# Kernel optimization log

Hardware: AMD Instinct MI355X
Metric: run time of the kernel (lower is better)

The kernel has to match this reference:

```python
import jax, jax.numpy as jnp
import numpy as np

N, EN, NNZ, D, H = 100000, 25000, 200000, 128, 4
F = D  # out_channels per head (out_channels == embed_dim)
NEG_SLOPE = 0.2


def segment_softmax(logits, seg, num_segments):
    # numerically stable softmax over entries sharing the same segment id
    m = jax.ops.segment_max(logits, seg, num_segments=num_segments)
    ex = jnp.exp(logits - m[seg])
    s = jax.ops.segment_sum(ex, seg, num_segments=num_segments)
    return ex / s[seg]


def setup_inputs():
    key = jax.random.key(0)
    ks = jax.random.split(key, 10)
    X = jax.random.normal(ks[0], (N, D), jnp.float32)
    E = jax.random.normal(ks[1], (EN, D), jnp.float32)
    row = jax.random.randint(ks[2], (NNZ,), 0, N, dtype=jnp.int32)
    col = (jnp.arange(NNZ, dtype=jnp.int32) % EN)  # every hyperedge non-empty
    adj_index = jnp.stack([row, col])  # [2, nnz]
    adj_values = jax.random.uniform(ks[3], (NNZ,), jnp.float32) + 0.1
    s = 1.0 / np.sqrt(D)
    Wn = jax.random.normal(ks[4], (D, D), jnp.float32) * s
    bn = jnp.zeros((D,), jnp.float32)
    We = jax.random.normal(ks[5], (D, D), jnp.float32) * s
    be = jnp.zeros((D,), jnp.float32)
    Wlin = jax.random.normal(ks[6], (D, H * F), jnp.float32) * s
    att = jax.random.normal(ks[7], (1, H, 2 * F), jnp.float32) * s
    bias_conv = jnp.zeros((F,), jnp.float32)
    return {"X": X, "E": E, "adj_index": adj_index, "adj_values": adj_values,
            "Wn": Wn, "bn": bn, "We": We, "be": be, "Wlin": Wlin,
            "att": att, "bias_conv": bias_conv}


def reference(X, E, adj_index, adj_values, Wn, bn, We, be, Wlin, att, bias_conv):
    row, col = adj_index[0], adj_index[1]  # node idx, hyperedge idx

    # ---- compute_edge_feat: E_res = B^{-1} A^T (X Wn + bn) + (E We + be) + E
    edge_deg = jax.ops.segment_sum(adj_values, col, num_segments=EN)  # tsp.sum(A,0)
    norm_factor = 1.0 / edge_deg  # edges guaranteed non-empty
    X_trans = X @ Wn + bn
    agg = jax.ops.segment_sum(adj_values[:, None] * X_trans[row], col, num_segments=EN)
    E_res = norm_factor[:, None] * agg + (E @ We + be) + E

    # ---- HypergraphConv(use_attention=True, heads=H, concat=False), eval (dropout off)
    x = (X @ Wlin).reshape(N, H, F)
    e = (E_res @ Wlin).reshape(EN, H, F)
    x_i = x[row]           # [nnz, H, F]
    e_j = e[col]           # [nnz, H, F]
    alpha = (x_i * att[:, :, :F]).sum(-1) + (e_j * att[:, :, F:]).sum(-1)  # [nnz, H]
    alpha = jax.nn.leaky_relu(alpha, NEG_SLOPE)
    alpha = segment_softmax(alpha, row, N)  # softmax grouped by node index

    # degree normalizations D (nodes) and B (hyperedges)
    Dn = jax.ops.segment_sum(adj_values[col], row, num_segments=N)
    Dn = jnp.where(Dn > 0, 1.0 / Dn, 0.0)
    Bn = jax.ops.segment_sum(jnp.ones((NNZ,), x.dtype), col, num_segments=EN)
    Bn = jnp.where(Bn > 0, 1.0 / Bn, 0.0)

    # node -> hyperedge aggregation
    m1 = Bn[col][:, None, None] * x_i * alpha[:, :, None]
    out_e = jax.ops.segment_sum(m1, col, num_segments=EN)  # [EN, H, F]
    # hyperedge -> node aggregation
    m2 = Dn[row][:, None, None] * out_e[col] * alpha[:, :, None]
    out_n = jax.ops.segment_sum(m2, row, num_segments=N)   # [N, H, F]

    X_res = out_n.mean(axis=1) + bias_conv  # concat=False -> mean over heads + bias
    return (X_res, E_res)
```

## Files before the change

kernel.cpp:

```cpp
#include <hip/hip_runtime.h>

#define NN 100000
#define ENUM 25000
#define NNZ_C 200000

typedef __attribute__((ext_vector_type(8))) short bf16x8;
typedef __attribute__((ext_vector_type(4))) float f32x4;

__device__ __forceinline__ float bf2f(unsigned short v) {
    return __uint_as_float(((unsigned)v) << 16);
}
__device__ __forceinline__ float blo(unsigned u) { return __uint_as_float(u << 16); }
__device__ __forceinline__ float bhi(unsigned u) { return __uint_as_float(u & 0xFFFF0000u); }
__device__ __forceinline__ unsigned short f2bf(float x) {
    unsigned u = __float_as_uint(x);
    unsigned r = (u + 0x7fff + ((u >> 16) & 1)) >> 16;
    return (unsigned short)r;
}
__device__ __forceinline__ unsigned pack2(float a, float b) {
    return (unsigned)f2bf(a) | ((unsigned)f2bf(b) << 16);
}
__device__ __forceinline__ void gload_lds16(const unsigned short* g, unsigned short* l) {
    __builtin_amdgcn_global_load_lds(
        (const __attribute__((address_space(1))) void*)g,
        (__attribute__((address_space(3))) void*)l, 16, 0, 0);
}

template <bool PERM>
__global__ __launch_bounds__(256) void wtr_k(
    const float* __restrict__ W, unsigned short* __restrict__ Wt, int NC)
{
    const int t = blockIdx.x * 256 + threadIdx.x;
    if (t >= 128 * NC) return;
    const int c = t % NC, k = t / NC;
    const int cc = PERM ? ((c & 127) * 4 + (c >> 7)) : c;
    const size_t pos = ((size_t)cc * 128 + k) ^ ((cc & 7) << 3);
    Wt[pos] = f2bf(W[t]);
}

__global__ __launch_bounds__(256) void attw_k(
    const float* __restrict__ Wlin, const float* __restrict__ att,
    float* __restrict__ A1, float* __restrict__ A2)
{
    const int t = threadIdx.x;
    const int k = t & 127;
    const int pair = t >> 7;
    const float* wrow = Wlin + (size_t)k * 512;
    float s[4];
    #pragma unroll
    for (int h = 0; h < 4; h++) {
        float acc = 0.f;
        const float* ap = att + h * 256 + pair * 128;
        const float* wp = wrow + h * 128;
        for (int f = 0; f < 128; f++) acc += wp[f] * ap[f];
        s[h] = acc;
    }
    float* dst = (pair ? A2 : A1) + k * 4;
    dst[0] = s[0]; dst[1] = s[1]; dst[2] = s[2]; dst[3] = s[3];
}

__global__ __launch_bounds__(256) void gemmx_k(
    const float* __restrict__ X, const unsigned short* __restrict__ Wc,
    const float* __restrict__ bn, const float* __restrict__ A1,
    unsigned short* __restrict__ Xt, unsigned short* __restrict__ Xlin,
    float* __restrict__ ax, int M)
{
    __shared__ unsigned short As[64 * 128];
    __shared__ unsigned short Bs[64 * 128];
    __shared__ float A1s[512];
    const int tid = threadIdx.x;
    const int r0 = blockIdx.x * 64;

    {
        int rr = tid >> 4;
        const int kc = (tid & 15) * 8;
        #pragma unroll
        for (int it = 0; it < 4; it++) {
            int r = r0 + rr; if (r > M - 1) r = M - 1;
            const float* ap = X + (size_t)r * 128 + kc;
            const float4 f0 = *(const float4*)ap;
            const float4 f1 = *(const float4*)(ap + 4);
            uint4 va;
            va.x = pack2(f0.x, f0.y); va.y = pack2(f0.z, f0.w);
            va.z = pack2(f1.x, f1.y); va.w = pack2(f1.z, f1.w);
            *(uint4*)&As[(rr * 128 + kc) ^ ((rr & 7) << 3)] = va;
            rr += 16;
        }
    }
    A1s[tid] = A1[tid];
    A1s[tid + 256] = A1[tid + 256];
    __syncthreads();

    {
        const int rr = tid >> 2;
        const int fq = (tid & 3) * 32;
        float s0 = 0.f, s1 = 0.f, s2 = 0.f, s3 = 0.f;
        #pragma unroll
        for (int i = 0; i < 32; i += 8) {
            const bf16x8 v = *(const bf16x8*)&As[(rr * 128 + fq + i) ^ ((rr & 7) << 3)];
            #pragma unroll
            for (int j = 0; j < 8; j++) {
                const float xv = bf2f((unsigned short)v[j]);
                const float* ap = A1s + (fq + i + j) * 4;
                s0 += xv * ap[0]; s1 += xv * ap[1];
                s2 += xv * ap[2]; s3 += xv * ap[3];
            }
        }
        s0 += __shfl_xor(s0, 1); s1 += __shfl_xor(s1, 1);
        s2 += __shfl_xor(s2, 1); s3 += __shfl_xor(s3, 1);
        s0 += __shfl_xor(s0, 2); s1 += __shfl_xor(s1, 2);
        s2 += __shfl_xor(s2, 2); s3 += __shfl_xor(s3, 2);
        const int r = r0 + rr;
        if ((tid & 3) == 0 && r < M)
            *(float4*)(ax + (size_t)r * 4) = make_float4(s0, s1, s2, s3);
    }

    const int lane = tid & 63;
    const int wid = tid >> 6;
    const int wr = wid >> 1, wc = wid & 1;
    const int fr = lane & 15;
    const int kg = (lane >> 4) * 8;

    bf16x8 a[2][4];
    #pragma unroll
    for (int m = 0; m < 2; m++) {
        const int ar = wr * 32 + m * 16 + fr;
        #pragma unroll
        for (int ks = 0; ks < 4; ks++)
            a[m][ks] = *(const bf16x8*)&As[(ar * 128 + ks * 32 + kg) ^ ((ar & 7) << 3)];
    }

    for (int ct = 0; ct < 10; ct++) {
        __syncthreads();
        {
            const unsigned short* src = Wc + (size_t)ct * 8192 + tid * 8;
            unsigned short* dst = &Bs[tid * 8];
            #pragma unroll
            for (int it = 0; it < 4; it++)
                gload_lds16(src + it * 2048, dst + it * 2048);
        }
        __syncthreads();

        f32x4 acc[2][2] = {};
        #pragma unroll
        for (int ks = 0; ks < 4; ks++) {
            bf16x8 b[2];
            #pragma unroll
            for (int n = 0; n < 2; n++) {
                const int br = wc * 32 + n * 16 + fr;
                b[n] = *(const bf16x8*)&Bs[(br * 128 + ks * 32 + kg) ^ ((br & 7) << 3)];
            }
            #pragma unroll
            for (int m = 0; m < 2; m++)
                #pragma unroll
                for (int n = 0; n < 2; n++)
                    acc[m][n] = __builtin_amdgcn_mfma_f32_16x16x32_bf16(a[m][ks], b[n], acc[m][n], 0, 0, 0);
        }

        #pragma unroll
        for (int m = 0; m < 2; m++) {
            #pragma unroll
            for (int n = 0; n < 2; n++) {
                const int ccol = wc * 32 + n * 16 + fr;
                #pragma unroll
                for (int j = 0; j < 4; j++) {
                    const int r = r0 + wr * 32 + m * 16 + (lane >> 4) * 4 + j;
                    if (r < M) {
                        const float v = acc[m][n][j];
                        if (ct < 2) {
                            const int c = ct * 64 + ccol;
                            Xt[(size_t)r * 128 + c] = f2bf(v + bn[c]);
                        } else {
                            const int c = (ct - 2) * 64 + ccol;
                            Xlin[(size_t)r * 512 + c] = f2bf(v);
                        }
                    }
                }
            }
        }
    }
}

template <bool BF16OUT, int CT, bool AF32>
__global__ __launch_bounds__(256) void gemm2_k(
    const void* __restrict__ Av, const unsigned short* __restrict__ Wt,
    const float* __restrict__ bias, const float* __restrict__ resid,
    void* __restrict__ Cv, int M)
{
    const int NC = CT * 64;
    __shared__ unsigned short As[64 * 128];
    __shared__ unsigned short Bs[64 * 128];
    const int tid = threadIdx.x;
    const int r0 = blockIdx.x * 64;

    {
        int rr = tid >> 4;
        const int kc = (tid & 15) * 8;
        #pragma unroll
        for (int it = 0; it < 4; it++) {
            int r = r0 + rr; if (r > M - 1) r = M - 1;
            uint4 va;
            if (AF32) {
                const float* ap = (const float*)Av + (size_t)r * 128 + kc;
                const float4 f0 = *(const float4*)ap;
                const float4 f1 = *(const float4*)(ap + 4);
                va.x = pack2(f0.x, f0.y); va.y = pack2(f0.z, f0.w);
                va.z = pack2(f1.x, f1.y); va.w = pack2(f1.z, f1.w);
            } else {
                va = *(const uint4*)((const unsigned short*)Av + (size_t)r * 128 + kc);
            }
            *(uint4*)&As[(rr * 128 + kc) ^ ((rr & 7) << 3)] = va;
            rr += 16;
        }
    }
    __syncthreads();

    const int lane = tid & 63;
    const int wid = tid >> 6;
    const int wr = wid >> 1, wc = wid & 1;
    const int fr = lane & 15;
    const int kg = (lane >> 4) * 8;

    bf16x8 a[2][4];
    #pragma unroll
    for (int m = 0; m < 2; m++) {
        const int ar = wr * 32 + m * 16 + fr;
        #pragma unroll
        for (int ks = 0; ks < 4; ks++)
            a[m][ks] = *(const bf16x8*)&As[(ar * 128 + ks * 32 + kg) ^ ((ar & 7) << 3)];
    }

    for (int ct = 0; ct < CT; ct++) {
        __syncthreads();
        {
            const unsigned short* src = Wt + (size_t)ct * 8192 + tid * 8;
            unsigned short* dst = &Bs[tid * 8];
            #pragma unroll
            for (int it = 0; it < 4; it++)
                gload_lds16(src + it * 2048, dst + it * 2048);
        }
        __syncthreads();

        f32x4 acc[2][2] = {};
        #pragma unroll
        for (int ks = 0; ks < 4; ks++) {
            bf16x8 b[2];
            #pragma unroll
            for (int n = 0; n < 2; n++) {
                const int br = wc * 32 + n * 16 + fr;
                b[n] = *(const bf16x8*)&Bs[(br * 128 + ks * 32 + kg) ^ ((br & 7) << 3)];
            }
            #pragma unroll
            for (int m = 0; m < 2; m++)
                #pragma unroll
                for (int n = 0; n < 2; n++)
                    acc[m][n] = __builtin_amdgcn_mfma_f32_16x16x32_bf16(a[m][ks], b[n], acc[m][n], 0, 0, 0);
        }

        const int c0 = ct * 64;
        #pragma unroll
        for (int m = 0; m < 2; m++) {
            #pragma unroll
            for (int n = 0; n < 2; n++) {
                const int c = c0 + wc * 32 + n * 16 + (lane & 15);
                #pragma unroll
                for (int j = 0; j < 4; j++) {
                    const int r = r0 + wr * 32 + m * 16 + (lane >> 4) * 4 + j;
                    if (r < M) {
                        float v = acc[m][n][j];
                        if (bias) v += bias[c];
                        if (resid) v += resid[(size_t)r * NC + c];
                        if (BF16OUT) ((unsigned short*)Cv)[(size_t)r * NC + c] = f2bf(v);
                        else         ((float*)Cv)[(size_t)r * NC + c] = v;
                    }
                }
            }
        }
    }
}

__global__ __launch_bounds__(256) void edge_agg_k(
    const int* __restrict__ row, const float* __restrict__ adjv,
    const unsigned short* __restrict__ Xt, const float* __restrict__ A2,
    float* __restrict__ Eres, float* __restrict__ ae)
{
    __shared__ float part[4][4];
    const int s = threadIdx.x >> 7;
    const int e = blockIdx.x * 2 + s;
    const int f = threadIdx.x & 127;
    float v = 0.f;
    if (e < ENUM) {
        float acc = 0.f, deg = 0.f;
        #pragma unroll
        for (int j = 0; j < 8; j++) {
            const int k = e + j * ENUM;
            const float w = adjv[k];
            deg += w;
            acc += w * blo(Xt[(size_t)row[k] * 128 + f]);
        }
        v = Eres[(size_t)e * 128 + f] + acc / deg;
        Eres[(size_t)e * 128 + f] = v;
    }
    const float4 a2 = *(const float4*)(A2 + f * 4);
    float p0 = v * a2.x, p1 = v * a2.y, p2 = v * a2.z, p3 = v * a2.w;
    #pragma unroll
    for (int off = 1; off < 64; off <<= 1) {
        p0 += __shfl_xor(p0, off); p1 += __shfl_xor(p1, off);
        p2 += __shfl_xor(p2, off); p3 += __shfl_xor(p3, off);
    }
    const int w = threadIdx.x >> 6;
    if ((threadIdx.x & 63) == 0) {
        part[w][0] = p0; part[w][1] = p1; part[w][2] = p2; part[w][3] = p3;
    }
    __syncthreads();
    if ((threadIdx.x & 127) == 0 && e < ENUM) {
        float4 o;
        o.x = part[2 * s][0] + part[2 * s + 1][0];
        o.y = part[2 * s][1] + part[2 * s + 1][1];
        o.z = part[2 * s][2] + part[2 * s + 1][2];
        o.w = part[2 * s][3] + part[2 * s + 1][3];
        *(float4*)(ae + (size_t)e * 4) = o;
    }
}

__global__ __launch_bounds__(256) void zero_k(unsigned* __restrict__ p, int n)
{
    const int t = blockIdx.x * 256 + threadIdx.x;
    if (t < n) p[t] = 0u;
}

__global__ __launch_bounds__(256) void hist_k(
    const int* __restrict__ row, int* __restrict__ cnt)
{
    const int k = blockIdx.x * 256 + threadIdx.x;
    if (k < NNZ_C) atomicAdd(cnt + row[k], 1);
}

__global__ __launch_bounds__(256) void scan1_k(
    const int* __restrict__ cnt, int* __restrict__ rp, int* __restrict__ bsum, int n)
{
    __shared__ int sh[256];
    const int t = threadIdx.x, g = blockIdx.x * 256 + t;
    const int v = (g < n) ? cnt[g] : 0;
    sh[t] = v; __syncthreads();
    #pragma unroll
    for (int off = 1; off < 256; off <<= 1) {
        const int add = (t >= off) ? sh[t - off] : 0;
        __syncthreads();
        sh[t] += add;
        __syncthreads();
    }
    if (g < n) rp[g] = sh[t] - v;
    if (t == 255) bsum[blockIdx.x] = sh[255];
}

__global__ __launch_bounds__(512) void scan2_k(int* __restrict__ bsum, int nb)
{
    __shared__ int sh[512];
    const int t = threadIdx.x;
    const int v = (t < nb) ? bsum[t] : 0;
    sh[t] = v; __syncthreads();
    #pragma unroll
    for (int off = 1; off < 512; off <<= 1) {
        const int add = (t >= off) ? sh[t - off] : 0;
        __syncthreads();
        sh[t] += add;
        __syncthreads();
    }
    if (t < nb) bsum[t] = sh[t] - v;
}

__global__ __launch_bounds__(256) void scan3_k(
    int* __restrict__ rp, const int* __restrict__ bsum, int* __restrict__ cur, int n)
{
    const int g = blockIdx.x * 256 + threadIdx.x;
    if (g < n) {
        const int v = rp[g] + bsum[g >> 8];
        rp[g] = v;
        cur[g] = v;
    }
    if (g == 0) rp[n] = NNZ_C;
}

__global__ __launch_bounds__(256) void fill_k(
    const int* __restrict__ row, int* __restrict__ cur, int* __restrict__ eidx)
{
    const int k = blockIdx.x * 256 + threadIdx.x;
    if (k < NNZ_C) {
        const int p = atomicAdd(cur + row[k], 1);
        eidx[p] = k;
    }
}

__global__ __launch_bounds__(256) void softmax_csr_k(
    const int* __restrict__ rowptr, const int* __restrict__ eidx,
    const float* __restrict__ ax, const float* __restrict__ ae,
    float* __restrict__ alpha)
{
    const int t = blockIdx.x * 256 + threadIdx.x;
    if (t >= NN * 4) return;
    const int r = t >> 2, h = t & 3;
    const int p0 = rowptr[r], p1 = rowptr[r + 1];
    if (p0 == p1) return;
    const float axv = ax[t];
    float m = -1e30f;
    for (int p = p0; p < p1; ++p) {
        const int c = eidx[p] % ENUM;
        float a = axv + ae[c * 4 + h];
        a = (a >= 0.f) ? a : 0.2f * a;
        m = fmaxf(m, a);
    }
    float s = 0.f;
    for (int p = p0; p < p1; ++p) {
        const int c = eidx[p] % ENUM;
        float a = axv + ae[c * 4 + h];
        a = (a >= 0.f) ? a : 0.2f * a;
        s += __expf(a - m);
    }
    const float rs = 1.f / s;
    for (int p = p0; p < p1; ++p) {
        const int k = eidx[p];
        const int c = k % ENUM;
        float a = axv + ae[c * 4 + h];
        a = (a >= 0.f) ? a : 0.2f * a;
        alpha[(size_t)k * 4 + h] = __expf(a - m) * rs;
    }
}

__global__ __launch_bounds__(256) void out_e_k(
    const int* __restrict__ row, const float* __restrict__ alpha,
    const unsigned short* __restrict__ Xlin, unsigned short* __restrict__ out_e)
{
    const int e = blockIdx.x * 4 + (threadIdx.x >> 6);
    const int lane = threadIdx.x & 63;
    if (e >= ENUM) return;
    const int f0 = lane * 2;
    float a0 = 0.f, a1 = 0.f, a2 = 0.f, a3 = 0.f;
    float a4 = 0.f, a5 = 0.f, a6 = 0.f, a7 = 0.f;
    #pragma unroll
    for (int j = 0; j < 8; j++) {
        const int k = e + j * ENUM;
        const int r = row[k];
        const float4 al = *(const float4*)(alpha + (size_t)k * 4);
        const uint4 u = *(const uint4*)(Xlin + (size_t)r * 512 + f0 * 4);
        a0 += al.x * blo(u.x); a1 += al.y * bhi(u.x);
        a2 += al.z * blo(u.y); a3 += al.w * bhi(u.y);
        a4 += al.x * blo(u.z); a5 += al.y * bhi(u.z);
        a6 += al.z * blo(u.w); a7 += al.w * bhi(u.w);
    }
    uint4 o;
    o.x = pack2(0.125f * a0, 0.125f * a1);
    o.y = pack2(0.125f * a2, 0.125f * a3);
    o.z = pack2(0.125f * a4, 0.125f * a5);
    o.w = pack2(0.125f * a6, 0.125f * a7);
    *(uint4*)(out_e + (size_t)e * 512 + f0 * 4) = o;
}

__global__ __launch_bounds__(256) void xgather_k(
    const int* __restrict__ rowptr, const int* __restrict__ eidx,
    const float* __restrict__ adjv, const float* __restrict__ alpha,
    const unsigned short* __restrict__ out_e, const float* __restrict__ bias,
    float* __restrict__ Xres)
{
    const int r = blockIdx.x * 4 + (threadIdx.x >> 6);
    const int lane = threadIdx.x & 63;
    if (r >= NN) return;
    const int p0 = rowptr[r], p1 = rowptr[r + 1];
    const int f0 = lane * 2;
    float a0 = 0.f, a1 = 0.f, ds = 0.f;

#define XG_BODY(P) {                                                          \
        const int k = eidx[P];                                                \
        const int c = k % ENUM;                                               \
        ds += adjv[c];                                                        \
        const float4 al = *(const float4*)(alpha + ((size_t)k << 2));         \
        const uint4 u = *(const uint4*)(out_e + (size_t)c * 512 + f0 * 4);    \
        a0 += al.x * blo(u.x) + al.y * bhi(u.x) + al.z * blo(u.y) + al.w * bhi(u.y); \
        a1 += al.x * blo(u.z) + al.y * bhi(u.z) + al.z * blo(u.w) + al.w * bhi(u.w); \
    }

    int p = p0;
    for (; p + 2 <= p1; p += 2) { XG_BODY(p); XG_BODY(p + 1); }
    if (p < p1) XG_BODY(p);
#undef XG_BODY

    const float w = (p1 > p0) ? 0.25f / ds : 0.f;
    float2 o;
    o.x = bias[f0] + w * a0;
    o.y = bias[f0 + 1] + w * a1;
    *(float2*)(Xres + (size_t)r * 128 + f0) = o;
}

extern "C" void kernel_launch(void* const* d_in, const int* in_sizes, int n_in,
                              void* d_out, int out_size, void* d_ws, size_t ws_size,
                              hipStream_t stream)
{
    const float* X         = (const float*)d_in[0];
    const float* E         = (const float*)d_in[1];
    const int*   adj       = (const int*)d_in[2];
    const float* adjv      = (const float*)d_in[3];
    const float* Wn        = (const float*)d_in[4];
    const float* bn        = (const float*)d_in[5];
    const float* We        = (const float*)d_in[6];
    const float* be        = (const float*)d_in[7];
    const float* Wlin      = (const float*)d_in[8];
    const float* att       = (const float*)d_in[9];
    const float* bias_conv = (const float*)d_in[10];
    const int* row = adj;

    float* Xres = (float*)d_out;
    float* Eres = Xres + (size_t)NN * 128;

    char* wsb = (char*)d_ws;
    unsigned short* out_e = (unsigned short*)(wsb);
    unsigned short* Xt    = (unsigned short*)(wsb + 25600000);
    unsigned short* Xlin  = (unsigned short*)(wsb + 51200000);
    unsigned short* Wcomb = (unsigned short*)(wsb + 153600000);
    unsigned short* WeT   = (unsigned short*)(wsb + 153763840);
    float* A1    = (float*)(wsb + 153796608);
    float* A2    = (float*)(wsb + 153798656);
    float* ax    = (float*)(wsb + 153800704);
    float* ae    = (float*)(wsb + 155400704);
    float* alpha = (float*)(wsb + 155800704);
    int* rowptr  = (int*)(wsb + 159000704);
    int* cnt     = (int*)(wsb + 159400720);
    int* eidx    = (int*)(wsb + 159800720);
    int* bsum    = (int*)(wsb + 160600720);

    zero_k<<<(NN + 255) / 256, 256, 0, stream>>>((unsigned*)cnt, NN);
    hist_k<<<(NNZ_C + 255) / 256, 256, 0, stream>>>(row, cnt);
    scan1_k<<<(NN + 255) / 256, 256, 0, stream>>>(cnt, rowptr, bsum, NN);
    scan2_k<<<1, 512, 0, stream>>>(bsum, (NN + 255) / 256);
    scan3_k<<<(NN + 255) / 256, 256, 0, stream>>>(rowptr, bsum, cnt, NN);
    fill_k<<<(NNZ_C + 255) / 256, 256, 0, stream>>>(row, cnt, eidx);

    wtr_k<false><<<64, 256, 0, stream>>>(Wn, Wcomb, 128);
    wtr_k<true><<<256, 256, 0, stream>>>(Wlin, Wcomb + 128 * 128, 512);
    wtr_k<false><<<64, 256, 0, stream>>>(We, WeT, 128);
    attw_k<<<1, 256, 0, stream>>>(Wlin, att, A1, A2);

    gemmx_k<<<1563, 256, 0, stream>>>(X, Wcomb, bn, A1, Xt, Xlin, ax, NN);

    gemm2_k<false, 2, true><<<391, 256, 0, stream>>>(E, WeT, be, E, Eres, ENUM);
    edge_agg_k<<<ENUM / 2, 256, 0, stream>>>(row, adjv, Xt, A2, Eres, ae);

    softmax_csr_k<<<(NN * 4) / 256 + 1, 256, 0, stream>>>(rowptr, eidx, ax, ae, alpha);

    out_e_k<<<ENUM / 4, 256, 0, stream>>>(row, alpha, Xlin, out_e);

    xgather_k<<<NN / 4, 256, 0, stream>>>(rowptr, eidx, adjv, alpha, out_e, bias_conv, Xres);
}
```

Baseline: 232.9 us.

## Aggregate raw X per hyperedge before applying Wn, fusing with E GEMM

Uses linearity to compute the normalized hyperedge aggregation of raw X first and then multiply by Wn, instead of transforming all N nodes by Wn. This removes the 128-column Xt output from the big node GEMM and the 25.6MB Xt write/read. The Wn and We products are fused into one dual-MFMA GEMM over hyperedges, with the bias sum precomputed. Attention logits for edges move to a separate small kernel, which adds a launch and an extra read of Eres. Rounding the aggregate to bf16 also changes the numerics slightly.

```diff
diff --git a/kernel.cpp b/kernel.cpp
--- a/kernel.cpp
+++ b/kernel.cpp
@@ -40,7 +40,8 @@
 
 __global__ __launch_bounds__(256) void attw_k(
     const float* __restrict__ Wlin, const float* __restrict__ att,
-    float* __restrict__ A1, float* __restrict__ A2)
+    const float* __restrict__ bn, const float* __restrict__ be,
+    float* __restrict__ A1, float* __restrict__ A2, float* __restrict__ bnbe)
 {
     const int t = threadIdx.x;
     const int k = t & 127;
@@ -57,13 +58,13 @@
     }
     float* dst = (pair ? A2 : A1) + k * 4;
     dst[0] = s[0]; dst[1] = s[1]; dst[2] = s[2]; dst[3] = s[3];
+    if (t < 128) bnbe[t] = bn[t] + be[t];
 }
 
 __global__ __launch_bounds__(256) void gemmx_k(
-    const float* __restrict__ X, const unsigned short* __restrict__ Wc,
-    const float* __restrict__ bn, const float* __restrict__ A1,
-    unsigned short* __restrict__ Xt, unsigned short* __restrict__ Xlin,
-    float* __restrict__ ax, int M)
+    const float* __restrict__ X, const unsigned short* __restrict__ Wlp,
+    const float* __restrict__ A1,
+    unsigned short* __restrict__ Xlin, float* __restrict__ ax, int M)
 {
     __shared__ unsigned short As[64 * 128];
     __shared__ unsigned short Bs[64 * 128];
@@ -130,10 +131,10 @@
             a[m][ks] = *(const bf16x8*)&As[(ar * 128 + ks * 32 + kg) ^ ((ar & 7) << 3)];
     }
 
-    for (int ct = 0; ct < 10; ct++) {
+    for (int ct = 0; ct < 8; ct++) {
         __syncthreads();
         {
-            const unsigned short* src = Wc + (size_t)ct * 8192 + tid * 8;
+            const unsigned short* src = Wlp + (size_t)ct * 8192 + tid * 8;
             unsigned short* dst = &Bs[tid * 8];
             #pragma unroll
             for (int it = 0; it < 4; it++)
@@ -161,35 +162,48 @@
         for (int m = 0; m < 2; m++) {
             #pragma unroll
             for (int n = 0; n < 2; n++) {
-                const int ccol = wc * 32 + n * 16 + fr;
+                const int c = ct * 64 + wc * 32 + n * 16 + fr;
                 #pragma unroll
                 for (int j = 0; j < 4; j++) {
                     const int r = r0 + wr * 32 + m * 16 + (lane >> 4) * 4 + j;
-                    if (r < M) {
-                        const float v = acc[m][n][j];
-                        if (ct < 2) {
-                            const int c = ct * 64 + ccol;
-                            Xt[(size_t)r * 128 + c] = f2bf(v + bn[c]);
-                        } else {
-                            const int c = (ct - 2) * 64 + ccol;
-                            Xlin[(size_t)r * 512 + c] = f2bf(v);
-                        }
-                    }
+                    if (r < M)
+                        Xlin[(size_t)r * 512 + c] = f2bf(acc[m][n][j]);
                 }
             }
         }
     }
 }
 
-template <bool BF16OUT, int CT, bool AF32>
-__global__ __launch_bounds__(256) void gemm2_k(
-    const void* __restrict__ Av, const unsigned short* __restrict__ Wt,
-    const float* __restrict__ bias, const float* __restrict__ resid,
-    void* __restrict__ Cv, int M)
-{
-    const int NC = CT * 64;
-    __shared__ unsigned short As[64 * 128];
-    __shared__ unsigned short Bs[64 * 128];
+__global__ __launch_bounds__(256) void agg_k(
+    const int* __restrict__ row, const float* __restrict__ adjv,
+    const float* __restrict__ X, unsigned short* __restrict__ agg)
+{
+    const int e = blockIdx.x * 4 + (threadIdx.x >> 6);
+    const int lane = threadIdx.x & 63;
+    if (e >= ENUM) return;
+    const int f0 = lane * 2;
+    float a0 = 0.f, a1 = 0.f, deg = 0.f;
+    #pragma unroll
+    for (int j = 0; j < 8; j++) {
+        const int k = e + j * ENUM;
+        const float w = adjv[k];
+        deg += w;
+        const float2 x = *(const float2*)(X + (size_t)row[k] * 128 + f0);
+        a0 += w * x.x; a1 += w * x.y;
+    }
+    const float rs = 1.f / deg;
+    ((unsigned*)agg)[(size_t)e * 64 + lane] = pack2(a0 * rs, a1 * rs);
+}
+
+__global__ __launch_bounds__(256) void gemme_k(
+    const unsigned short* __restrict__ agg, const float* __restrict__ E,
+    const unsigned short* __restrict__ WnT, const unsigned short* __restrict__ WeT,
+    const float* __restrict__ bnbe, float* __restrict__ Eres, int M)
+{
+    __shared__ unsigned short Ag[64 * 128];
+    __shared__ unsigned short Ae[64 * 128];
+    __shared__ unsigned short Bw[64 * 128];
+    __shared__ unsigned short Bv[64 * 128];
     const int tid = threadIdx.x;
     const int r0 = blockIdx.x * 64;
 
@@ -199,17 +213,16 @@
         #pragma unroll
         for (int it = 0; it < 4; it++) {
             int r = r0 + rr; if (r > M - 1) r = M - 1;
-            uint4 va;
-            if (AF32) {
-                const float* ap = (const float*)Av + (size_t)r * 128 + kc;
-                const float4 f0 = *(const float4*)ap;
-                const float4 f1 = *(const float4*)(ap + 4);
-                va.x = pack2(f0.x, f0.y); va.y = pack2(f0.z, f0.w);
-                va.z = pack2(f1.x, f1.y); va.w = pack2(f1.z, f1.w);
-            } else {
-                va = *(const uint4*)((const unsigned short*)Av + (size_t)r * 128 + kc);
-            }
-            *(uint4*)&As[(rr * 128 + kc) ^ ((rr & 7) << 3)] = va;
+            const uint4 vg = *(const uint4*)(agg + (size_t)r * 128 + kc);
+            const float* ep = E + (size_t)r * 128 + kc;
+            const float4 f0 = *(const float4*)ep;
+            const float4 f1 = *(const float4*)(ep + 4);
+            uint4 ve;
+            ve.x = pack2(f0.x, f0.y); ve.y = pack2(f0.z, f0.w);
+            ve.z = pack2(f1.x, f1.y); ve.w = pack2(f1.z, f1.w);
+            const int idx = (rr * 128 + kc) ^ ((rr & 7) << 3);
+            *(uint4*)&Ag[idx] = vg;
+            *(uint4*)&Ae[idx] = ve;
             rr += 16;
         }
     }
@@ -221,106 +234,90 @@
     const int fr = lane & 15;
     const int kg = (lane >> 4) * 8;
 
-    bf16x8 a[2][4];
+    bf16x8 ag[2][4], ae_[2][4];
     #pragma unroll
     for (int m = 0; m < 2; m++) {
         const int ar = wr * 32 + m * 16 + fr;
         #pragma unroll
-        for (int ks = 0; ks < 4; ks++)
-            a[m][ks] = *(const bf16x8*)&As[(ar * 128 + ks * 32 + kg) ^ ((ar & 7) << 3)];
-    }
-
-    for (int ct = 0; ct < CT; ct++) {
+        for (int ks = 0; ks < 4; ks++) {
+            const int idx = (ar * 128 + ks * 32 + kg) ^ ((ar & 7) << 3);
+            ag[m][ks] = *(const bf16x8*)&Ag[idx];
+            ae_[m][ks] = *(const bf16x8*)&Ae[idx];
+        }
+    }
+
+    for (int ct = 0; ct < 2; ct++) {
         __syncthreads();
         {
-            const unsigned short* src = Wt + (size_t)ct * 8192 + tid * 8;
-            unsigned short* dst = &Bs[tid * 8];
-            #pragma unroll
-            for (int it = 0; it < 4; it++)
-                gload_lds16(src + it * 2048, dst + it * 2048);
+            const unsigned short* s1 = WnT + (size_t)ct * 8192 + tid * 8;
+            const unsigned short* s2 = WeT + (size_t)ct * 8192 + tid * 8;
+            unsigned short* d1 = &Bw[tid * 8];
+            unsigned short* d2 = &Bv[tid * 8];
+            #pragma unroll
+            for (int it = 0; it < 4; it++) {
+                gload_lds16(s1 + it * 2048, d1 + it * 2048);
+                gload_lds16(s2 + it * 2048, d2 + it * 2048);
+            }
         }
         __syncthreads();
 
         f32x4 acc[2][2] = {};
         #pragma unroll
         for (int ks = 0; ks < 4; ks++) {
-            bf16x8 b[2];
+            bf16x8 bw[2], bv[2];
             #pragma unroll
             for (int n = 0; n < 2; n++) {
                 const int br = wc * 32 + n * 16 + fr;
-                b[n] = *(const bf16x8*)&Bs[(br * 128 + ks * 32 + kg) ^ ((br & 7) << 3)];
+                const int idx = (br * 128 + ks * 32 + kg) ^ ((br & 7) << 3);
+                bw[n] = *(const bf16x8*)&Bw[idx];
+                bv[n] = *(const bf16x8*)&Bv[idx];
             }
             #pragma unroll
             for (int m = 0; m < 2; m++)
                 #pragma unroll
-                for (int n = 0; n < 2; n++)
-                    acc[m][n] = __builtin_amdgcn_mfma_f32_16x16x32_bf16(a[m][ks], b[n], acc[m][n], 0, 0, 0);
-        }
-
-        const int c0 = ct * 64;
+                for (int n = 0; n < 2; n++) {
+                    acc[m][n] = __builtin_amdgcn_mfma_f32_16x16x32_bf16(ag[m][ks], bw[n], acc[m][n], 0, 0, 0);
+                    acc[m][n] = __builtin_amdgcn_mfma_f32_16x16x32_bf16(ae_[m][ks], bv[n], acc[m][n], 0, 0, 0);
+                }
+        }
+
         #pragma unroll
         for (int m = 0; m < 2; m++) {
             #pragma unroll
             for (int n = 0; n < 2; n++) {
-                const int c = c0 + wc * 32 + n * 16 + (lane & 15);
+                const int c = ct * 64 + wc * 32 + n * 16 + fr;
                 #pragma unroll
                 for (int j = 0; j < 4; j++) {
                     const int r = r0 + wr * 32 + m * 16 + (lane >> 4) * 4 + j;
-                    if (r < M) {
-                        float v = acc[m][n][j];
-                        if (bias) v += bias[c];
-                        if (resid) v += resid[(size_t)r * NC + c];
-                        if (BF16OUT) ((unsigned short*)Cv)[(size_t)r * NC + c] = f2bf(v);
-                        else         ((float*)Cv)[(size_t)r * NC + c] = v;
-                    }
+                    if (r < M)
+                        Eres[(size_t)r * 128 + c] = acc[m][n][j] + bnbe[c] + E[(size_t)r * 128 + c];
                 }
             }
         }
     }
 }
 
-__global__ __launch_bounds__(256) void edge_agg_k(
-    const int* __restrict__ row, const float* __restrict__ adjv,
-    const unsigned short* __restrict__ Xt, const float* __restrict__ A2,
-    float* __restrict__ Eres, float* __restrict__ ae)
-{
-    __shared__ float part[4][4];
-    const int s = threadIdx.x >> 7;
-    const int e = blockIdx.x * 2 + s;
-    const int f = threadIdx.x & 127;
-    float v = 0.f;
-    if (e < ENUM) {
-        float acc = 0.f, deg = 0.f;
-        #pragma unroll
-        for (int j = 0; j < 8; j++) {
-            const int k = e + j * ENUM;
-            const float w = adjv[k];
-            deg += w;
-            acc += w * blo(Xt[(size_t)row[k] * 128 + f]);
-        }
-        v = Eres[(size_t)e * 128 + f] + acc / deg;
-        Eres[(size_t)e * 128 + f] = v;
-    }
-    const float4 a2 = *(const float4*)(A2 + f * 4);
-    float p0 = v * a2.x, p1 = v * a2.y, p2 = v * a2.z, p3 = v * a2.w;
+__global__ __launch_bounds__(256) void ae_k(
+    const float* __restrict__ Eres, const float* __restrict__ A2,
+    float* __restrict__ ae)
+{
+    const int e = blockIdx.x * 4 + (threadIdx.x >> 6);
+    const int lane = threadIdx.x & 63;
+    if (e >= ENUM) return;
+    const int f0 = lane * 2;
+    const float2 v = *(const float2*)(Eres + (size_t)e * 128 + f0);
+    const float4 a0 = *(const float4*)(A2 + f0 * 4);
+    const float4 a1 = *(const float4*)(A2 + f0 * 4 + 4);
+    float s0 = v.x * a0.x + v.y * a1.x;
+    float s1 = v.x * a0.y + v.y * a1.y;
+    float s2 = v.x * a0.z + v.y * a1.z;
+    float s3 = v.x * a0.w + v.y * a1.w;
     #pragma unroll
     for (int off = 1; off < 64; off <<= 1) {
-        p0 += __shfl_xor(p0, off); p1 += __shfl_xor(p1, off);
-        p2 += __shfl_xor(p2, off); p3 += __shfl_xor(p3, off);
-    }
-    const int w = threadIdx.x >> 6;
-    if ((threadIdx.x & 63) == 0) {
-        part[w][0] = p0; part[w][1] = p1; part[w][2] = p2; part[w][3] = p3;
-    }
-    __syncthreads();
-    if ((threadIdx.x & 127) == 0 && e < ENUM) {
-        float4 o;
-        o.x = part[2 * s][0] + part[2 * s + 1][0];
-        o.y = part[2 * s][1] + part[2 * s + 1][1];
-        o.z = part[2 * s][2] + part[2 * s + 1][2];
-        o.w = part[2 * s][3] + part[2 * s + 1][3];
-        *(float4*)(ae + (size_t)e * 4) = o;
-    }
+        s0 += __shfl_xor(s0, off); s1 += __shfl_xor(s1, off);
+        s2 += __shfl_xor(s2, off); s3 += __shfl_xor(s3, off);
+    }
+    if (lane == 0) *(float4*)(ae + (size_t)e * 4) = make_float4(s0, s1, s2, s3);
 }
 
 __global__ __launch_bounds__(256) void zero_k(unsigned* __restrict__ p, int n)
@@ -513,19 +510,21 @@
 
     char* wsb = (char*)d_ws;
     unsigned short* out_e = (unsigned short*)(wsb);
-    unsigned short* Xt    = (unsigned short*)(wsb + 25600000);
+    unsigned short* agg   = (unsigned short*)(wsb + 25600000);
     unsigned short* Xlin  = (unsigned short*)(wsb + 51200000);
-    unsigned short* Wcomb = (unsigned short*)(wsb + 153600000);
+    unsigned short* Wlp   = (unsigned short*)(wsb + 153600000);
+    unsigned short* WnT   = (unsigned short*)(wsb + 153731072);
     unsigned short* WeT   = (unsigned short*)(wsb + 153763840);
     float* A1    = (float*)(wsb + 153796608);
     float* A2    = (float*)(wsb + 153798656);
-    float* ax    = (float*)(wsb + 153800704);
-    float* ae    = (float*)(wsb + 155400704);
-    float* alpha = (float*)(wsb + 155800704);
-    int* rowptr  = (int*)(wsb + 159000704);
-    int* cnt     = (int*)(wsb + 159400720);
-    int* eidx    = (int*)(wsb + 159800720);
-    int* bsum    = (int*)(wsb + 160600720);
+    float* bnbe  = (float*)(wsb + 153800704);
+    float* ax    = (float*)(wsb + 153802752);
+    float* ae    = (float*)(wsb + 155402752);
+    float* alpha = (float*)(wsb + 155802752);
+    int* rowptr  = (int*)(wsb + 159002752);
+    int* cnt     = (int*)(wsb + 159402768);
+    int* eidx    = (int*)(wsb + 159802768);
+    int* bsum    = (int*)(wsb + 160602768);
 
     zero_k<<<(NN + 255) / 256, 256, 0, stream>>>((unsigned*)cnt, NN);
     hist_k<<<(NNZ_C + 255) / 256, 256, 0, stream>>>(row, cnt);
@@ -534,15 +533,16 @@
     scan3_k<<<(NN + 255) / 256, 256, 0, stream>>>(rowptr, bsum, cnt, NN);
     fill_k<<<(NNZ_C + 255) / 256, 256, 0, stream>>>(row, cnt, eidx);
 
-    wtr_k<false><<<64, 256, 0, stream>>>(Wn, Wcomb, 128);
-    wtr_k<true><<<256, 256, 0, stream>>>(Wlin, Wcomb + 128 * 128, 512);
+    wtr_k<true><<<256, 256, 0, stream>>>(Wlin, Wlp, 512);
+    wtr_k<false><<<64, 256, 0, stream>>>(Wn, WnT, 128);
     wtr_k<false><<<64, 256, 0, stream>>>(We, WeT, 128);
-    attw_k<<<1, 256, 0, stream>>>(Wlin, att, A1, A2);
-
-    gemmx_k<<<1563, 256, 0, stream>>>(X, Wcomb, bn, A1, Xt, Xlin, ax, NN);
-
-    gemm2_k<false, 2, true><<<391, 256, 0, stream>>>(E, WeT, be, E, Eres, ENUM);
-    edge_agg_k<<<ENUM / 2, 256, 0, stream>>>(row, adjv, Xt, A2, Eres, ae);
+    attw_k<<<1, 256, 0, stream>>>(Wlin, att, bn, be, A1, A2, bnbe);
+
+    gemmx_k<<<1563, 256, 0, stream>>>(X, Wlp, A1, Xlin, ax, NN);
+
+    agg_k<<<ENUM / 4, 256, 0, stream>>>(row, adjv, X, agg);
+    gemme_k<<<391, 256, 0, stream>>>(agg, E, WnT, WeT, bnbe, Eres, ENUM);
+    ae_k<<<ENUM / 4, 256, 0, stream>>>(Eres, A2, ae);
 
     softmax_csr_k<<<(NN * 4) / 256 + 1, 256, 0, stream>>>(rowptr, eidx, ax, ae, alpha);
 
```

New measurement: 227.5 us. -2.3%, faster.
